# Kernel tuning notes

Measured on AMD Instinct MI355X. Metric: run time of the kernel, lower is better.

## Reference

```python
import jax, jax.numpy as jnp
import numpy as np

B, LMAX, NCOND, NHID = 256, 512, 300, 600

def setup_inputs() -> dict:
    key = jax.random.key(0)
    ks = jax.random.split(key, 7)
    x = jax.random.normal(ks[0], (B, NCOND), dtype=jnp.float32)
    context = jax.random.normal(ks[1], (B, LMAX, NCOND), dtype=jnp.float32)
    lengths = jax.random.randint(ks[2], (B,), 0, LMAX, dtype=jnp.int32)
    W1 = jax.random.normal(ks[3], (NCOND, NHID), dtype=jnp.float32) * (1.0 / np.sqrt(NCOND))
    b1 = jax.random.normal(ks[4], (NHID,), dtype=jnp.float32) * 0.02
    Wa = jax.random.normal(ks[5], (NHID, NCOND), dtype=jnp.float32) * (1.0 / np.sqrt(NHID))
    ba = jax.random.normal(ks[6], (NCOND,), dtype=jnp.float32) * 0.02
    return {"x": x, "context": context, "lengths": lengths, "W1": W1, "b1": b1, "Wa": Wa, "ba": ba}

def reference(x, context, lengths, W1, b1, Wa, ba):
    # lengths clamped to >=1 (a ragged context is always non-empty)
    lens = jnp.maximum(lengths, 1)
    # valid-position mask over padded context: [B, L, 1]
    valid = (jnp.arange(LMAX)[None, :] < lens[:, None])[..., None].astype(context.dtype)
    # per-token MLP: relu(ctx @ W1 + b1)  -> [B, L, nhid]
    h = jax.nn.relu(jnp.einsum('blc,ch->blh', context, W1) + b1)
    # masked mean over valid tokens (ragged mean-pool) -> [B, nhid]
    pooled = jnp.sum(h * valid, axis=1) / lens[:, None].astype(context.dtype)
    # sigmoid gate -> [B, ncond], applied to x embeddings
    gate = jax.nn.sigmoid(jnp.einsum('bh,hc->bc', pooled, Wa) + ba)
    return gate * x
```

## Files before the change

### kernel.cpp

```cpp
#include <hip/hip_runtime.h>
#include <math.h>

#define BB     256
#define LMAX   512
#define NCOND  300
#define NHID   600
#define NSEG   8
#define CHUNK  64
#define KPAD   320
#define KLDS   328
#define NKC    10

#define AS1 __attribute__((address_space(1)))
#define AS3 __attribute__((address_space(3)))

typedef short s16x8 __attribute__((ext_vector_type(8)));
typedef float f32x4 __attribute__((ext_vector_type(4)));
typedef unsigned short u16x4 __attribute__((ext_vector_type(4)));

__device__ inline unsigned short f2bf(float f) {
    unsigned int x = __float_as_uint(f);
    x += 0x7fffu + ((x >> 16) & 1u);
    return (unsigned short)(x >> 16);
}

__global__ __launch_bounds__(256) void k0_w1t(const float* __restrict__ W1,
                                              unsigned short* __restrict__ w1t)
{
    const int t     = blockIdx.x * 256 + threadIdx.x;
    const int lane  = t & 63;
    const int g     = t >> 6;
    const int ntile = g / NKC;
    const int kc    = g - ntile * NKC;
    const int n     = ntile * 16 + (lane & 15);
    const int kbase = kc * 32 + (lane >> 4) * 8;
    union { unsigned short us[8]; s16x8 v8; } u;
#pragma unroll
    for (int j = 0; j < 8; ++j) {
        const int k = kbase + j;
        const float w = (n < NHID && k < NCOND) ? W1[(size_t)k * NHID + n] : 0.f;
        u.us[j] = f2bf(w);
    }
    *(s16x8*)(w1t + (size_t)t * 8) = u.v8;
}

__global__ __launch_bounds__(256) void k0b_cvt(const float* __restrict__ ctx,
                                               const int* __restrict__ lengths,
                                               unsigned short* __restrict__ ctx16)
{
    const int b = blockIdx.x, s = blockIdx.y, tid = threadIdx.x;
    int count = lengths[b]; if (count < 1) count = 1;
    if (s * CHUNK >= count) return;

    const size_t inbase  = ((size_t)b * LMAX + s * CHUNK) * NCOND;
    const float* src = ctx + inbase;
    char* dst = (char*)(ctx16 + ((size_t)b * LMAX + s * CHUNK) * KPAD);

#pragma unroll
    for (int i = 0; i < 20; ++i) {
        const int c   = i * 256 + tid;
        const int row = c / 80;
        const int q   = c - row * 80;
        float4 v = make_float4(0.f, 0.f, 0.f, 0.f);
        if (q < 75)
            v = *(const float4*)(src + (size_t)row * NCOND + q * 4);
        union { unsigned short us[4]; u16x4 v4; } o;
        o.us[0] = f2bf(v.x); o.us[1] = f2bf(v.y);
        o.us[2] = f2bf(v.z); o.us[3] = f2bf(v.w);
        const int off = (row * 640 + q * 8) ^ ((row & 7) << 4);
        *(u16x4*)(dst + off) = o.v4;
    }
}

__global__ __launch_bounds__(256, 3) void k1_mfma_dma(
    const unsigned short* __restrict__ ctx16, const int* __restrict__ lengths,
    const unsigned short* __restrict__ w1t, const float* __restrict__ b1,
    float* __restrict__ partial)
{
    const int b  = blockIdx.x;
    const int s  = blockIdx.y;
    const int ch = blockIdx.z;

    int count = lengths[b]; if (count < 1) count = 1;
    const int l0 = s * CHUNK;
    if (l0 >= count) return;
    const int valid = min(count - l0, CHUNK);

    const int tid  = threadIdx.x;
    const int lane = tid & 63;
    const int wv   = tid >> 6;
    const int ln15 = lane & 15;
    const int kg   = lane >> 4;

    __shared__ __align__(16) unsigned short atile[CHUNK * KPAD];

    const char* gsrc = (const char*)(ctx16 + ((size_t)b * LMAX + l0) * KPAD);
    char* lbase = (char*)atile;
#pragma unroll
    for (int r = 0; r < 10; ++r) {
        const int off = (r * 4 + wv) * 1024;
        __builtin_amdgcn_global_load_lds(
            (const AS1 void*)(gsrc + off + lane * 16),
            (AS3 void*)(lbase + off),
            16, 0, 0);
    }

    const int ntile0 = ch * 20 + wv * 5;
    const unsigned short* bbase = w1t + ((size_t)ntile0 * NKC * 64 + lane) * 8;
    s16x8 bf[2][5];
#pragma unroll
    for (int nt = 0; nt < 5; ++nt) bf[0][nt] = *(const s16x8*)(bbase + nt * 5120);

    __syncthreads();

    const int swz   = (ln15 & 7) << 4;
    const int abase = ln15 * 640 + kg * 16;
    const char* ab  = (const char*)atile;

    f32x4 acc[5][4];
#pragma unroll
    for (int nt = 0; nt < 5; ++nt)
#pragma unroll
        for (int mt = 0; mt < 4; ++mt) acc[nt][mt] = (f32x4){0.f, 0.f, 0.f, 0.f};

#pragma unroll
    for (int kc = 0; kc < NKC; ++kc) {
        const int cur = kc & 1, nxt = cur ^ 1;
        if (kc < NKC - 1) {
#pragma unroll
            for (int nt = 0; nt < 5; ++nt)
                bf[nxt][nt] = *(const s16x8*)(bbase + nt * 5120 + (kc + 1) * 512);
        }
        s16x8 af[4];
#pragma unroll
        for (int mt = 0; mt < 4; ++mt)
            af[mt] = *(const s16x8*)(ab + ((abase + mt * 10240 + kc * 64) ^ swz));
#pragma unroll
        for (int nt = 0; nt < 5; ++nt)
#pragma unroll
            for (int mt = 0; mt < 4; ++mt)
                acc[nt][mt] = __builtin_amdgcn_mfma_f32_16x16x32_bf16(
                    af[mt], bf[cur][nt], acc[nt][mt], 0, 0, 0);
    }

#pragma unroll
    for (int nt = 0; nt < 5; ++nt) {
        const int colg = ch * 320 + wv * 80 + nt * 16 + ln15;
        const float b1c = (colg < NHID) ? b1[colg] : 0.f;
        float ssum = 0.f;
#pragma unroll
        for (int mt = 0; mt < 4; ++mt) {
            const int rbase = mt * 16 + kg * 4;
#pragma unroll
            for (int r = 0; r < 4; ++r) {
                const float h = fmaxf(acc[nt][mt][r] + b1c, 0.f);
                if (rbase + r < valid) ssum += h;
            }
        }
        ssum += __shfl_xor(ssum, 16, 64);
        ssum += __shfl_xor(ssum, 32, 64);
        if (kg == 0 && colg < NHID)
            partial[((size_t)s * BB + b) * NHID + colg] = ssum;
    }
}

__global__ __launch_bounds__(256, 3) void k1_mfma_pool(
    const float* __restrict__ ctx, const int* __restrict__ lengths,
    const unsigned short* __restrict__ w1t, const float* __restrict__ b1,
    float* __restrict__ partial)
{
    const int b  = blockIdx.x;
    const int s  = blockIdx.y;
    const int ch = blockIdx.z;

    int count = lengths[b]; if (count < 1) count = 1;
    const int l0 = s * CHUNK;
    if (l0 >= count) return;
    const int valid = min(count - l0, CHUNK);

    const int tid  = threadIdx.x;
    const int lane = tid & 63;
    const int wv   = tid >> 6;
    const int ln15 = lane & 15;
    const int kg   = lane >> 4;

    __shared__ __align__(16) unsigned short atile[CHUNK * KLDS];

#pragma unroll
    for (int p = 0; p < 10; ++p) {
        const int i  = p * 256 + tid;
        const int r  = i / 40;
        const int c8 = i - r * 40;
        union { unsigned short us[8]; s16x8 v8; } u;
        if (r < valid && c8 < 38) {
            const float* src = ctx + ((size_t)b * LMAX + l0 + r) * NCOND + c8 * 8;
            const float4 v0 = *(const float4*)src;
            float4 v1 = make_float4(0.f, 0.f, 0.f, 0.f);
            if (c8 < 37) v1 = *(const float4*)(src + 4);
            u.us[0] = f2bf(v0.x); u.us[1] = f2bf(v0.y);
            u.us[2] = f2bf(v0.z); u.us[3] = f2bf(v0.w);
            u.us[4] = f2bf(v1.x); u.us[5] = f2bf(v1.y);
            u.us[6] = f2bf(v1.z); u.us[7] = f2bf(v1.w);
        } else {
#pragma unroll
            for (int j = 0; j < 8; ++j) u.us[j] = 0;
        }
        *(s16x8*)(atile + r * KLDS + c8 * 8) = u.v8;
    }
    __syncthreads();

    const int ntile0 = ch * 20 + wv * 5;
    const unsigned short* bbase = w1t + ((size_t)ntile0 * NKC * 64 + lane) * 8;
    const unsigned short* arow  = atile + ln15 * KLDS + kg * 8;

    f32x4 acc[5][4];
#pragma unroll
    for (int nt = 0; nt < 5; ++nt)
#pragma unroll
        for (int mt = 0; mt < 4; ++mt) acc[nt][mt] = (f32x4){0.f, 0.f, 0.f, 0.f};

    s16x8 bf[2][5];
#pragma unroll
    for (int nt = 0; nt < 5; ++nt) bf[0][nt] = *(const s16x8*)(bbase + nt * 5120);

#pragma unroll
    for (int kc = 0; kc < NKC; ++kc) {
        const int cur = kc & 1, nxt = cur ^ 1;
        if (kc < NKC - 1) {
#pragma unroll
            for (int nt = 0; nt < 5; ++nt)
                bf[nxt][nt] = *(const s16x8*)(bbase + nt * 5120 + (kc + 1) * 512);
        }
        s16x8 af[4];
#pragma unroll
        for (int mt = 0; mt < 4; ++mt)
            af[mt] = *(const s16x8*)(arow + mt * 16 * KLDS + kc * 32);
#pragma unroll
        for (int nt = 0; nt < 5; ++nt)
#pragma unroll
            for (int mt = 0; mt < 4; ++mt)
                acc[nt][mt] = __builtin_amdgcn_mfma_f32_16x16x32_bf16(
                    af[mt], bf[cur][nt], acc[nt][mt], 0, 0, 0);
    }

#pragma unroll
    for (int nt = 0; nt < 5; ++nt) {
        const int colg = ch * 320 + wv * 80 + nt * 16 + ln15;
        const float b1c = (colg < NHID) ? b1[colg] : 0.f;
        float ssum = 0.f;
#pragma unroll
        for (int mt = 0; mt < 4; ++mt) {
            const int rbase = mt * 16 + kg * 4;
#pragma unroll
            for (int r = 0; r < 4; ++r) {
                const float h = fmaxf(acc[nt][mt][r] + b1c, 0.f);
                if (rbase + r < valid) ssum += h;
            }
        }
        ssum += __shfl_xor(ssum, 16, 64);
        ssum += __shfl_xor(ssum, 32, 64);
        if (kg == 0 && colg < NHID)
            partial[((size_t)s * BB + b) * NHID + colg] = ssum;
    }
}

__global__ __launch_bounds__(640) void k2_gate(
    const float* __restrict__ x, const int* __restrict__ lengths,
    const float* __restrict__ partial, const float* __restrict__ Wa,
    const float* __restrict__ ba, float* __restrict__ out)
{
    const int b0  = blockIdx.x * 2;
    const int tid = threadIdx.x;

    __shared__ float pl[2][NHID];

    if (tid < NHID) {
#pragma unroll
        for (int bb = 0; bb < 2; ++bb) {
            int count = lengths[b0 + bb]; if (count < 1) count = 1;
            const int nch = (count + CHUNK - 1) >> 6;
            float ssum = 0.f;
            for (int sp = 0; sp < nch; ++sp)
                ssum += partial[((size_t)sp * BB + (b0 + bb)) * NHID + tid];
            pl[bb][tid] = ssum / (float)count;
        }
    }
    __syncthreads();

    if (tid < 2 * NCOND) {
        const int bb = tid / NCOND;
        const int n  = tid - bb * NCOND;
        const int b  = b0 + bb;
        float a0 = ba[n], a1 = 0.f, a2 = 0.f, a3 = 0.f;
        const float4* p4 = (const float4*)pl[bb];
        for (int h4 = 0; h4 < 148; h4 += 4) {
            const float4 pv0 = p4[h4];
            const float4 pv1 = p4[h4 + 1];
            const float4 pv2 = p4[h4 + 2];
            const float4 pv3 = p4[h4 + 3];
            const int hb = h4 * 4;
            a0 = fmaf(pv0.x, Wa[(size_t)(hb +  0) * NCOND + n], a0);
            a0 = fmaf(pv0.y, Wa[(size_t)(hb +  1) * NCOND + n], a0);
            a0 = fmaf(pv0.z, Wa[(size_t)(hb +  2) * NCOND + n], a0);
            a0 = fmaf(pv0.w, Wa[(size_t)(hb +  3) * NCOND + n], a0);
            a1 = fmaf(pv1.x, Wa[(size_t)(hb +  4) * NCOND + n], a1);
            a1 = fmaf(pv1.y, Wa[(size_t)(hb +  5) * NCOND + n], a1);
            a1 = fmaf(pv1.z, Wa[(size_t)(hb +  6) * NCOND + n], a1);
            a1 = fmaf(pv1.w, Wa[(size_t)(hb +  7) * NCOND + n], a1);
            a2 = fmaf(pv2.x, Wa[(size_t)(hb +  8) * NCOND + n], a2);
            a2 = fmaf(pv2.y, Wa[(size_t)(hb +  9) * NCOND + n], a2);
            a2 = fmaf(pv2.z, Wa[(size_t)(hb + 10) * NCOND + n], a2);
            a2 = fmaf(pv2.w, Wa[(size_t)(hb + 11) * NCOND + n], a2);
            a3 = fmaf(pv3.x, Wa[(size_t)(hb + 12) * NCOND + n], a3);
            a3 = fmaf(pv3.y, Wa[(size_t)(hb + 13) * NCOND + n], a3);
            a3 = fmaf(pv3.z, Wa[(size_t)(hb + 14) * NCOND + n], a3);
            a3 = fmaf(pv3.w, Wa[(size_t)(hb + 15) * NCOND + n], a3);
        }
        {
            const float4 pv0 = p4[148];
            const float4 pv1 = p4[149];
            a0 = fmaf(pv0.x, Wa[(size_t)592 * NCOND + n], a0);
            a0 = fmaf(pv0.y, Wa[(size_t)593 * NCOND + n], a0);
            a0 = fmaf(pv0.z, Wa[(size_t)594 * NCOND + n], a0);
            a0 = fmaf(pv0.w, Wa[(size_t)595 * NCOND + n], a0);
            a1 = fmaf(pv1.x, Wa[(size_t)596 * NCOND + n], a1);
            a1 = fmaf(pv1.y, Wa[(size_t)597 * NCOND + n], a1);
            a1 = fmaf(pv1.z, Wa[(size_t)598 * NCOND + n], a1);
            a1 = fmaf(pv1.w, Wa[(size_t)599 * NCOND + n], a1);
        }
        const float acc  = (a0 + a1) + (a2 + a3);
        const float gate = 1.0f / (1.0f + expf(-acc));
        out[(size_t)b * NCOND + n] = gate * x[(size_t)b * NCOND + n];
    }
}

extern "C" void kernel_launch(void* const* d_in, const int* in_sizes, int n_in,
                              void* d_out, int out_size, void* d_ws, size_t ws_size,
                              hipStream_t stream)
{
    const float* x       = (const float*)d_in[0];
    const float* ctx     = (const float*)d_in[1];
    const int*   lengths = (const int*)  d_in[2];
    const float* W1      = (const float*)d_in[3];
    const float* b1      = (const float*)d_in[4];
    const float* Wa      = (const float*)d_in[5];
    const float* ba      = (const float*)d_in[6];
    float*       out     = (float*)d_out;

    const size_t W1T_B   = 409600;
    const size_t PART_B  = 4915200;
    const size_t CTX16_B = (size_t)BB * LMAX * KPAD * 2;
    const size_t NEED    = W1T_B + PART_B + CTX16_B;

    unsigned short* w1t     = (unsigned short*)d_ws;
    float*          partial = (float*)((char*)d_ws + W1T_B);

    k0_w1t<<<100, 256, 0, stream>>>(W1, w1t);

    if (ws_size >= NEED) {
        unsigned short* ctx16 = (unsigned short*)((char*)d_ws + W1T_B + PART_B);
        k0b_cvt<<<dim3(BB, NSEG), 256, 0, stream>>>(ctx, lengths, ctx16);
        k1_mfma_dma<<<dim3(BB, NSEG, 2), 256, 0, stream>>>(ctx16, lengths, w1t, b1, partial);
    } else {
        k1_mfma_pool<<<dim3(BB, NSEG, 2), 256, 0, stream>>>(ctx, lengths, w1t, b1, partial);
    }

    k2_gate<<<BB / 2, 640, 0, stream>>>(x, lengths, partial, Wa, ba, out);
}
```

Before: 309.5 us.

## Use one persistent block per batch with double-buffered segment DMA

Replaces the per-(batch, segment, column-half) MFMA kernel with a 512-thread block per batch row. Each block loops over that row's valid 64-token segments, prefetching the next bf16 segment into a second LDS buffer while it computes the current one, and keeps the pooled sums in registers. Because each block now writes only a single pooled vector, the partial buffer shrinks and the gate kernel no longer sums per-segment partials. The conversion kernel also switches to 8-wide loads and stores. The cost is far fewer blocks with uneven work: rows with long lengths run up to 8 segments serially, and W1 fragments are reloaded for every segment.

```diff
diff --git a/kernel.cpp b/kernel.cpp
--- a/kernel.cpp
+++ b/kernel.cpp
@@ -10,13 +10,14 @@
 #define KPAD   320
 #define KLDS   328
 #define NKC    10
+#define SEGB   (CHUNK * KPAD * 2)
 
 #define AS1 __attribute__((address_space(1)))
 #define AS3 __attribute__((address_space(3)))
 
 typedef short s16x8 __attribute__((ext_vector_type(8)));
 typedef float f32x4 __attribute__((ext_vector_type(4)));
-typedef unsigned short u16x4 __attribute__((ext_vector_type(4)));
+typedef unsigned short u16x8 __attribute__((ext_vector_type(8)));
 
 __device__ inline unsigned short f2bf(float f) {
     unsigned int x = __float_as_uint(f);
@@ -52,39 +53,37 @@
     int count = lengths[b]; if (count < 1) count = 1;
     if (s * CHUNK >= count) return;
 
-    const size_t inbase  = ((size_t)b * LMAX + s * CHUNK) * NCOND;
-    const float* src = ctx + inbase;
+    const float* src = ctx + ((size_t)b * LMAX + s * CHUNK) * NCOND;
     char* dst = (char*)(ctx16 + ((size_t)b * LMAX + s * CHUNK) * KPAD);
 
 #pragma unroll
-    for (int i = 0; i < 20; ++i) {
+    for (int i = 0; i < 10; ++i) {
         const int c   = i * 256 + tid;
-        const int row = c / 80;
-        const int q   = c - row * 80;
-        float4 v = make_float4(0.f, 0.f, 0.f, 0.f);
-        if (q < 75)
-            v = *(const float4*)(src + (size_t)row * NCOND + q * 4);
-        union { unsigned short us[4]; u16x4 v4; } o;
-        o.us[0] = f2bf(v.x); o.us[1] = f2bf(v.y);
-        o.us[2] = f2bf(v.z); o.us[3] = f2bf(v.w);
-        const int off = (row * 640 + q * 8) ^ ((row & 7) << 4);
-        *(u16x4*)(dst + off) = o.v4;
-    }
-}
-
-__global__ __launch_bounds__(256, 3) void k1_mfma_dma(
+        const int row = c / 40;
+        const int q2  = c - row * 40;
+        float4 v0 = make_float4(0.f, 0.f, 0.f, 0.f);
+        float4 v1 = make_float4(0.f, 0.f, 0.f, 0.f);
+        const float* rsrc = src + (size_t)row * NCOND + q2 * 8;
+        if (q2 < 38) v0 = *(const float4*)rsrc;
+        if (q2 < 37) v1 = *(const float4*)(rsrc + 4);
+        union { unsigned short us[8]; u16x8 v8; } o;
+        o.us[0] = f2bf(v0.x); o.us[1] = f2bf(v0.y);
+        o.us[2] = f2bf(v0.z); o.us[3] = f2bf(v0.w);
+        o.us[4] = f2bf(v1.x); o.us[5] = f2bf(v1.y);
+        o.us[6] = f2bf(v1.z); o.us[7] = f2bf(v1.w);
+        const int off = (row * 640 + q2 * 16) ^ ((row & 7) << 4);
+        *(u16x8*)(dst + off) = o.v8;
+    }
+}
+
+__global__ __launch_bounds__(512, 2) void k1_persist(
     const unsigned short* __restrict__ ctx16, const int* __restrict__ lengths,
     const unsigned short* __restrict__ w1t, const float* __restrict__ b1,
     float* __restrict__ partial)
 {
-    const int b  = blockIdx.x;
-    const int s  = blockIdx.y;
-    const int ch = blockIdx.z;
-
+    const int b = blockIdx.x;
     int count = lengths[b]; if (count < 1) count = 1;
-    const int l0 = s * CHUNK;
-    if (l0 >= count) return;
-    const int valid = min(count - l0, CHUNK);
+    const int nseg = (count + CHUNK - 1) >> 6;
 
     const int tid  = threadIdx.x;
     const int lane = tid & 63;
@@ -92,179 +91,109 @@
     const int ln15 = lane & 15;
     const int kg   = lane >> 4;
 
-    __shared__ __align__(16) unsigned short atile[CHUNK * KPAD];
-
-    const char* gsrc = (const char*)(ctx16 + ((size_t)b * LMAX + l0) * KPAD);
-    char* lbase = (char*)atile;
-#pragma unroll
-    for (int r = 0; r < 10; ++r) {
-        const int off = (r * 4 + wv) * 1024;
+    __shared__ __align__(16) unsigned short atile[2][CHUNK * KPAD];
+
+    float bq[5];
+#pragma unroll
+    for (int nt = 0; nt < 5; ++nt) {
+        const int colg = wv * 80 + nt * 16 + ln15;
+        bq[nt] = (colg < NHID) ? b1[colg] : 0.f;
+    }
+
+    const unsigned short* bbase = w1t + ((size_t)(wv * 5) * NKC * 64 + lane) * 8;
+    const char* gseg = (const char*)(ctx16 + (size_t)b * LMAX * KPAD);
+
+#pragma unroll
+    for (int r = 0; r < 5; ++r) {
+        const int off = (r * 8 + wv) * 1024;
         __builtin_amdgcn_global_load_lds(
-            (const AS1 void*)(gsrc + off + lane * 16),
-            (AS3 void*)(lbase + off),
-            16, 0, 0);
-    }
-
-    const int ntile0 = ch * 20 + wv * 5;
-    const unsigned short* bbase = w1t + ((size_t)ntile0 * NKC * 64 + lane) * 8;
-    s16x8 bf[2][5];
-#pragma unroll
-    for (int nt = 0; nt < 5; ++nt) bf[0][nt] = *(const s16x8*)(bbase + nt * 5120);
-
-    __syncthreads();
-
+            (const AS1 void*)(gseg + off + lane * 16),
+            (AS3 void*)((char*)atile[0] + off), 16, 0, 0);
+    }
+
+    float ssum[5] = {0.f, 0.f, 0.f, 0.f, 0.f};
     const int swz   = (ln15 & 7) << 4;
     const int abase = ln15 * 640 + kg * 16;
-    const char* ab  = (const char*)atile;
-
-    f32x4 acc[5][4];
-#pragma unroll
-    for (int nt = 0; nt < 5; ++nt)
-#pragma unroll
-        for (int mt = 0; mt < 4; ++mt) acc[nt][mt] = (f32x4){0.f, 0.f, 0.f, 0.f};
-
-#pragma unroll
-    for (int kc = 0; kc < NKC; ++kc) {
-        const int cur = kc & 1, nxt = cur ^ 1;
-        if (kc < NKC - 1) {
+
+    __syncthreads();
+
+    for (int s = 0; s < nseg; ++s) {
+        const int cur = s & 1;
+
+        if (s + 1 < nseg) {
+            const char* gnext = gseg + (size_t)(s + 1) * SEGB;
+#pragma unroll
+            for (int r = 0; r < 5; ++r) {
+                const int off = (r * 8 + wv) * 1024;
+                __builtin_amdgcn_global_load_lds(
+                    (const AS1 void*)(gnext + off + lane * 16),
+                    (AS3 void*)((char*)atile[cur ^ 1] + off), 16, 0, 0);
+            }
+        }
+
+        const char* ab = (const char*)atile[cur];
+
+        f32x4 acc[5][4];
+#pragma unroll
+        for (int nt = 0; nt < 5; ++nt)
+#pragma unroll
+            for (int mt = 0; mt < 4; ++mt) acc[nt][mt] = (f32x4){0.f, 0.f, 0.f, 0.f};
+
+        s16x8 bf[2][5];
+#pragma unroll
+        for (int nt = 0; nt < 5; ++nt) bf[0][nt] = *(const s16x8*)(bbase + nt * 5120);
+
+#pragma unroll
+        for (int kc = 0; kc < NKC; ++kc) {
+            const int curk = kc & 1, nxtk = curk ^ 1;
+            if (kc < NKC - 1) {
+#pragma unroll
+                for (int nt = 0; nt < 5; ++nt)
+                    bf[nxtk][nt] = *(const s16x8*)(bbase + nt * 5120 + (kc + 1) * 512);
+            }
+            s16x8 af[4];
+#pragma unroll
+            for (int mt = 0; mt < 4; ++mt)
+                af[mt] = *(const s16x8*)(ab + ((abase + mt * 10240 + kc * 64) ^ swz));
 #pragma unroll
             for (int nt = 0; nt < 5; ++nt)
-                bf[nxt][nt] = *(const s16x8*)(bbase + nt * 5120 + (kc + 1) * 512);
-        }
-        s16x8 af[4];
-#pragma unroll
-        for (int mt = 0; mt < 4; ++mt)
-            af[mt] = *(const s16x8*)(ab + ((abase + mt * 10240 + kc * 64) ^ swz));
-#pragma unroll
-        for (int nt = 0; nt < 5; ++nt)
-#pragma unroll
-            for (int mt = 0; mt < 4; ++mt)
-                acc[nt][mt] = __builtin_amdgcn_mfma_f32_16x16x32_bf16(
-                    af[mt], bf[cur][nt], acc[nt][mt], 0, 0, 0);
+#pragma unroll
+                for (int mt = 0; mt < 4; ++mt)
+                    acc[nt][mt] = __builtin_amdgcn_mfma_f32_16x16x32_bf16(
+                        af[mt], bf[curk][nt], acc[nt][mt], 0, 0, 0);
+        }
+
+        const int valid = min(count - s * CHUNK, CHUNK);
+#pragma unroll
+        for (int nt = 0; nt < 5; ++nt) {
+            float t = 0.f;
+#pragma unroll
+            for (int mt = 0; mt < 4; ++mt) {
+                const int rbase = mt * 16 + kg * 4;
+#pragma unroll
+                for (int r = 0; r < 4; ++r) {
+                    const float h = fmaxf(acc[nt][mt][r] + bq[nt], 0.f);
+                    if (rbase + r < valid) t += h;
+                }
+            }
+            ssum[nt] += t;
+        }
+
+        __syncthreads();
     }
 
 #pragma unroll
     for (int nt = 0; nt < 5; ++nt) {
-        const int colg = ch * 320 + wv * 80 + nt * 16 + ln15;
-        const float b1c = (colg < NHID) ? b1[colg] : 0.f;
-        float ssum = 0.f;
-#pragma unroll
-        for (int mt = 0; mt < 4; ++mt) {
-            const int rbase = mt * 16 + kg * 4;
-#pragma unroll
-            for (int r = 0; r < 4; ++r) {
-                const float h = fmaxf(acc[nt][mt][r] + b1c, 0.f);
-                if (rbase + r < valid) ssum += h;
-            }
-        }
-        ssum += __shfl_xor(ssum, 16, 64);
-        ssum += __shfl_xor(ssum, 32, 64);
+        float v = ssum[nt];
+        v += __shfl_xor(v, 16, 64);
+        v += __shfl_xor(v, 32, 64);
+        const int colg = wv * 80 + nt * 16 + ln15;
         if (kg == 0 && colg < NHID)
-            partial[((size_t)s * BB + b) * NHID + colg] = ssum;
-    }
-}
-
-__global__ __launch_bounds__(256, 3) void k1_mfma_pool(
-    const float* __restrict__ ctx, const int* __restrict__ lengths,
-    const unsigned short* __restrict__ w1t, const float* __restrict__ b1,
-    float* __restrict__ partial)
-{
-    const int b  = blockIdx.x;
-    const int s  = blockIdx.y;
-    const int ch = blockIdx.z;
-
-    int count = lengths[b]; if (count < 1) count = 1;
-    const int l0 = s * CHUNK;
-    if (l0 >= count) return;
-    const int valid = min(count - l0, CHUNK);
-
-    const int tid  = threadIdx.x;
-    const int lane = tid & 63;
-    const int wv   = tid >> 6;
-    const int ln15 = lane & 15;
-    const int kg   = lane >> 4;
-
-    __shared__ __align__(16) unsigned short atile[CHUNK * KLDS];
-
-#pragma unroll
-    for (int p = 0; p < 10; ++p) {
-        const int i  = p * 256 + tid;
-        const int r  = i / 40;
-        const int c8 = i - r * 40;
-        union { unsigned short us[8]; s16x8 v8; } u;
-        if (r < valid && c8 < 38) {
-            const float* src = ctx + ((size_t)b * LMAX + l0 + r) * NCOND + c8 * 8;
-            const float4 v0 = *(const float4*)src;
-            float4 v1 = make_float4(0.f, 0.f, 0.f, 0.f);
-            if (c8 < 37) v1 = *(const float4*)(src + 4);
-            u.us[0] = f2bf(v0.x); u.us[1] = f2bf(v0.y);
-            u.us[2] = f2bf(v0.z); u.us[3] = f2bf(v0.w);
-            u.us[4] = f2bf(v1.x); u.us[5] = f2bf(v1.y);
-            u.us[6] = f2bf(v1.z); u.us[7] = f2bf(v1.w);
-        } else {
-#pragma unroll
-            for (int j = 0; j < 8; ++j) u.us[j] = 0;
-        }
-        *(s16x8*)(atile + r * KLDS + c8 * 8) = u.v8;
-    }
-    __syncthreads();
-
-    const int ntile0 = ch * 20 + wv * 5;
-    const unsigned short* bbase = w1t + ((size_t)ntile0 * NKC * 64 + lane) * 8;
-    const unsigned short* arow  = atile + ln15 * KLDS + kg * 8;
-
-    f32x4 acc[5][4];
-#pragma unroll
-    for (int nt = 0; nt < 5; ++nt)
-#pragma unroll
-        for (int mt = 0; mt < 4; ++mt) acc[nt][mt] = (f32x4){0.f, 0.f, 0.f, 0.f};
-
-    s16x8 bf[2][5];
-#pragma unroll
-    for (int nt = 0; nt < 5; ++nt) bf[0][nt] = *(const s16x8*)(bbase + nt * 5120);
-
-#pragma unroll
-    for (int kc = 0; kc < NKC; ++kc) {
-        const int cur = kc & 1, nxt = cur ^ 1;
-        if (kc < NKC - 1) {
-#pragma unroll
-            for (int nt = 0; nt < 5; ++nt)
-                bf[nxt][nt] = *(const s16x8*)(bbase + nt * 5120 + (kc + 1) * 512);
-        }
-        s16x8 af[4];
-#pragma unroll
-        for (int mt = 0; mt < 4; ++mt)
-            af[mt] = *(const s16x8*)(arow + mt * 16 * KLDS + kc * 32);
-#pragma unroll
-        for (int nt = 0; nt < 5; ++nt)
-#pragma unroll
-            for (int mt = 0; mt < 4; ++mt)
-                acc[nt][mt] = __builtin_amdgcn_mfma_f32_16x16x32_bf16(
-                    af[mt], bf[cur][nt], acc[nt][mt], 0, 0, 0);
-    }
-
-#pragma unroll
-    for (int nt = 0; nt < 5; ++nt) {
-        const int colg = ch * 320 + wv * 80 + nt * 16 + ln15;
-        const float b1c = (colg < NHID) ? b1[colg] : 0.f;
-        float ssum = 0.f;
-#pragma unroll
-        for (int mt = 0; mt < 4; ++mt) {
-            const int rbase = mt * 16 + kg * 4;
-#pragma unroll
-            for (int r = 0; r < 4; ++r) {
-                const float h = fmaxf(acc[nt][mt][r] + b1c, 0.f);
-                if (rbase + r < valid) ssum += h;
-            }
-        }
-        ssum += __shfl_xor(ssum, 16, 64);
-        ssum += __shfl_xor(ssum, 32, 64);
-        if (kg == 0 && colg < NHID)
-            partial[((size_t)s * BB + b) * NHID + colg] = ssum;
-    }
-}
-
-__global__ __launch_bounds__(640) void k2_gate(
+            partial[(size_t)b * NHID + colg] = v;
+    }
+}
+
+__global__ __launch_bounds__(640) void k2_gate2(
     const float* __restrict__ x, const int* __restrict__ lengths,
     const float* __restrict__ partial, const float* __restrict__ Wa,
     const float* __restrict__ ba, float* __restrict__ out)
@@ -278,11 +207,7 @@
 #pragma unroll
         for (int bb = 0; bb < 2; ++bb) {
             int count = lengths[b0 + bb]; if (count < 1) count = 1;
-            const int nch = (count + CHUNK - 1) >> 6;
-            float ssum = 0.f;
-            for (int sp = 0; sp < nch; ++sp)
-                ssum += partial[((size_t)sp * BB + (b0 + bb)) * NHID + tid];
-            pl[bb][tid] = ssum / (float)count;
+            pl[bb][tid] = partial[(size_t)(b0 + bb) * NHID + tid] / (float)count;
         }
     }
     __syncthreads();
@@ -334,6 +259,176 @@
     }
 }
 
+__global__ __launch_bounds__(256, 3) void k1_mfma_pool(
+    const float* __restrict__ ctx, const int* __restrict__ lengths,
+    const unsigned short* __restrict__ w1t, const float* __restrict__ b1,
+    float* __restrict__ partial)
+{
+    const int b  = blockIdx.x;
+    const int s  = blockIdx.y;
+    const int ch = blockIdx.z;
+
+    int count = lengths[b]; if (count < 1) count = 1;
+    const int l0 = s * CHUNK;
+    if (l0 >= count) return;
+    const int valid = min(count - l0, CHUNK);
+
+    const int tid  = threadIdx.x;
+    const int lane = tid & 63;
+    const int wv   = tid >> 6;
+    const int ln15 = lane & 15;
+    const int kg   = lane >> 4;
+
+    __shared__ __align__(16) unsigned short atile[CHUNK * KLDS];
+
+#pragma unroll
+    for (int p = 0; p < 10; ++p) {
+        const int i  = p * 256 + tid;
+        const int r  = i / 40;
+        const int c8 = i - r * 40;
+        union { unsigned short us[8]; s16x8 v8; } u;
+        if (r < valid && c8 < 38) {
+            const float* src = ctx + ((size_t)b * LMAX + l0 + r) * NCOND + c8 * 8;
+            const float4 v0 = *(const float4*)src;
+            float4 v1 = make_float4(0.f, 0.f, 0.f, 0.f);
+            if (c8 < 37) v1 = *(const float4*)(src + 4);
+            u.us[0] = f2bf(v0.x); u.us[1] = f2bf(v0.y);
+            u.us[2] = f2bf(v0.z); u.us[3] = f2bf(v0.w);
+            u.us[4] = f2bf(v1.x); u.us[5] = f2bf(v1.y);
+            u.us[6] = f2bf(v1.z); u.us[7] = f2bf(v1.w);
+        } else {
+#pragma unroll
+            for (int j = 0; j < 8; ++j) u.us[j] = 0;
+        }
+        *(s16x8*)(atile + r * KLDS + c8 * 8) = u.v8;
+    }
+    __syncthreads();
+
+    const int ntile0 = ch * 20 + wv * 5;
+    const unsigned short* bbase = w1t + ((size_t)ntile0 * NKC * 64 + lane) * 8;
+    const unsigned short* arow  = atile + ln15 * KLDS + kg * 8;
+
+    f32x4 acc[5][4];
+#pragma unroll
+    for (int nt = 0; nt < 5; ++nt)
+#pragma unroll
+        for (int mt = 0; mt < 4; ++mt) acc[nt][mt] = (f32x4){0.f, 0.f, 0.f, 0.f};
+
+    s16x8 bf[2][5];
+#pragma unroll
+    for (int nt = 0; nt < 5; ++nt) bf[0][nt] = *(const s16x8*)(bbase + nt * 5120);
+
+#pragma unroll
+    for (int kc = 0; kc < NKC; ++kc) {
+        const int cur = kc & 1, nxt = cur ^ 1;
+        if (kc < NKC - 1) {
+#pragma unroll
+            for (int nt = 0; nt < 5; ++nt)
+                bf[nxt][nt] = *(const s16x8*)(bbase + nt * 5120 + (kc + 1) * 512);
+        }
+        s16x8 af[4];
+#pragma unroll
+        for (int mt = 0; mt < 4; ++mt)
+            af[mt] = *(const s16x8*)(arow + mt * 16 * KLDS + kc * 32);
+#pragma unroll
+        for (int nt = 0; nt < 5; ++nt)
+#pragma unroll
+            for (int mt = 0; mt < 4; ++mt)
+                acc[nt][mt] = __builtin_amdgcn_mfma_f32_16x16x32_bf16(
+                    af[mt], bf[cur][nt], acc[nt][mt], 0, 0, 0);
+    }
+
+#pragma unroll
+    for (int nt = 0; nt < 5; ++nt) {
+        const int colg = ch * 320 + wv * 80 + nt * 16 + ln15;
+        const float b1c = (colg < NHID) ? b1[colg] : 0.f;
+        float ssum = 0.f;
+#pragma unroll
+        for (int mt = 0; mt < 4; ++mt) {
+            const int rbase = mt * 16 + kg * 4;
+#pragma unroll
+            for (int r = 0; r < 4; ++r) {
+                const float h = fmaxf(acc[nt][mt][r] + b1c, 0.f);
+                if (rbase + r < valid) ssum += h;
+            }
+        }
+        ssum += __shfl_xor(ssum, 16, 64);
+        ssum += __shfl_xor(ssum, 32, 64);
+        if (kg == 0 && colg < NHID)
+            partial[((size_t)s * BB + b) * NHID + colg] = ssum;
+    }
+}
+
+__global__ __launch_bounds__(640) void k2_gate(
+    const float* __restrict__ x, const int* __restrict__ lengths,
+    const float* __restrict__ partial, const float* __restrict__ Wa,
+    const float* __restrict__ ba, float* __restrict__ out)
+{
+    const int b0  = blockIdx.x * 2;
+    const int tid = threadIdx.x;
+
+    __shared__ float pl[2][NHID];
+
+    if (tid < NHID) {
+#pragma unroll
+        for (int bb = 0; bb < 2; ++bb) {
+            int count = lengths[b0 + bb]; if (count < 1) count = 1;
+            const int nch = (count + CHUNK - 1) >> 6;
+            float ssum = 0.f;
+            for (int sp = 0; sp < nch; ++sp)
+                ssum += partial[((size_t)sp * BB + (b0 + bb)) * NHID + tid];
+            pl[bb][tid] = ssum / (float)count;
+        }
+    }
+    __syncthreads();
+
+    if (tid < 2 * NCOND) {
+        const int bb = tid / NCOND;
+        const int n  = tid - bb * NCOND;
+        const int b  = b0 + bb;
+        float a0 = ba[n], a1 = 0.f, a2 = 0.f, a3 = 0.f;
+        const float4* p4 = (const float4*)pl[bb];
+        for (int h4 = 0; h4 < 148; h4 += 4) {
+            const float4 pv0 = p4[h4];
+            const float4 pv1 = p4[h4 + 1];
+            const float4 pv2 = p4[h4 + 2];
+            const float4 pv3 = p4[h4 + 3];
+            const int hb = h4 * 4;
+            a0 = fmaf(pv0.x, Wa[(size_t)(hb +  0) * NCOND + n], a0);
+            a0 = fmaf(pv0.y, Wa[(size_t)(hb +  1) * NCOND + n], a0);
+            a0 = fmaf(pv0.z, Wa[(size_t)(hb +  2) * NCOND + n], a0);
+            a0 = fmaf(pv0.w, Wa[(size_t)(hb +  3) * NCOND + n], a0);
+            a1 = fmaf(pv1.x, Wa[(size_t)(hb +  4) * NCOND + n], a1);
+            a1 = fmaf(pv1.y, Wa[(size_t)(hb +  5) * NCOND + n], a1);
+            a1 = fmaf(pv1.z, Wa[(size_t)(hb +  6) * NCOND + n], a1);
+            a1 = fmaf(pv1.w, Wa[(size_t)(hb +  7) * NCOND + n], a1);
+            a2 = fmaf(pv2.x, Wa[(size_t)(hb +  8) * NCOND + n], a2);
+            a2 = fmaf(pv2.y, Wa[(size_t)(hb +  9) * NCOND + n], a2);
+            a2 = fmaf(pv2.z, Wa[(size_t)(hb + 10) * NCOND + n], a2);
+            a2 = fmaf(pv2.w, Wa[(size_t)(hb + 11) * NCOND + n], a2);
+            a3 = fmaf(pv3.x, Wa[(size_t)(hb + 12) * NCOND + n], a3);
+            a3 = fmaf(pv3.y, Wa[(size_t)(hb + 13) * NCOND + n], a3);
+            a3 = fmaf(pv3.z, Wa[(size_t)(hb + 14) * NCOND + n], a3);
+            a3 = fmaf(pv3.w, Wa[(size_t)(hb + 15) * NCOND + n], a3);
+        }
+        {
+            const float4 pv0 = p4[148];
+            const float4 pv1 = p4[149];
+            a0 = fmaf(pv0.x, Wa[(size_t)592 * NCOND + n], a0);
+            a0 = fmaf(pv0.y, Wa[(size_t)593 * NCOND + n], a0);
+            a0 = fmaf(pv0.z, Wa[(size_t)594 * NCOND + n], a0);
+            a0 = fmaf(pv0.w, Wa[(size_t)595 * NCOND + n], a0);
+            a1 = fmaf(pv1.x, Wa[(size_t)596 * NCOND + n], a1);
+            a1 = fmaf(pv1.y, Wa[(size_t)597 * NCOND + n], a1);
+            a1 = fmaf(pv1.z, Wa[(size_t)598 * NCOND + n], a1);
+            a1 = fmaf(pv1.w, Wa[(size_t)599 * NCOND + n], a1);
+        }
+        const float acc  = (a0 + a1) + (a2 + a3);
+        const float gate = 1.0f / (1.0f + expf(-acc));
+        out[(size_t)b * NCOND + n] = gate * x[(size_t)b * NCOND + n];
+    }
+}
+
 extern "C" void kernel_launch(void* const* d_in, const int* in_sizes, int n_in,
                               void* d_out, int out_size, void* d_ws, size_t ws_size,
                               hipStream_t stream)
@@ -348,7 +443,7 @@
     float*       out     = (float*)d_out;
 
     const size_t W1T_B   = 409600;
-    const size_t PART_B  = 4915200;
+    const size_t PART_B  = 614400;
     const size_t CTX16_B = (size_t)BB * LMAX * KPAD * 2;
     const size_t NEED    = W1T_B + PART_B + CTX16_B;
 
@@ -360,10 +455,10 @@
     if (ws_size >= NEED) {
         unsigned short* ctx16 = (unsigned short*)((char*)d_ws + W1T_B + PART_B);
         k0b_cvt<<<dim3(BB, NSEG), 256, 0, stream>>>(ctx, lengths, ctx16);
-        k1_mfma_dma<<<dim3(BB, NSEG, 2), 256, 0, stream>>>(ctx16, lengths, w1t, b1, partial);
+        k1_persist<<<BB, 512, 0, stream>>>(ctx16, lengths, w1t, b1, partial);
+        k2_gate2<<<BB / 2, 640, 0, stream>>>(x, lengths, partial, Wa, ba, out);
     } else {
         k1_mfma_pool<<<dim3(BB, NSEG, 2), 256, 0, stream>>>(ctx, lengths, w1t, b1, partial);
-    }
-
-    k2_gate<<<BB / 2, 640, 0, stream>>>(x, lengths, partial, Wa, ba, out);
-}
+        k2_gate<<<BB / 2, 640, 0, stream>>>(x, lengths, partial, Wa, ba, out);
+    }
+}
```

Measured after the change: 379.9 us. 22.8% more time.

## Pre-swizzle context into MFMA fragment layout and load A directly from global

Applied to the files above, without the earlier changes.

The conversion kernel now writes bf16 context in the exact per-lane MFMA fragment order, so the GEMM kernel can load A operands straight from global memory into registers with double buffering. This drops the LDS staging, the async global-to-LDS copy and the block barrier. The grid order is changed so the two column-half blocks of one (batch, segment) tile run next to each other and can share the tile through L2, and launch bounds drop to 2 blocks per SIMD to leave room for the extra A registers. The cost is more global/L2 traffic per wave and lower occupancy.

```diff
diff --git a/kernel.cpp b/kernel.cpp
--- a/kernel.cpp
+++ b/kernel.cpp
@@ -10,13 +10,11 @@
 #define KPAD   320
 #define KLDS   328
 #define NKC    10
-
-#define AS1 __attribute__((address_space(1)))
-#define AS3 __attribute__((address_space(3)))
+#define TILE16 20480
 
 typedef short s16x8 __attribute__((ext_vector_type(8)));
 typedef float f32x4 __attribute__((ext_vector_type(4)));
-typedef unsigned short u16x4 __attribute__((ext_vector_type(4)));
+typedef unsigned short u16x8 __attribute__((ext_vector_type(8)));
 
 __device__ inline unsigned short f2bf(float f) {
     unsigned int x = __float_as_uint(f);
@@ -44,42 +42,46 @@
     *(s16x8*)(w1t + (size_t)t * 8) = u.v8;
 }
 
-__global__ __launch_bounds__(256) void k0b_cvt(const float* __restrict__ ctx,
-                                               const int* __restrict__ lengths,
-                                               unsigned short* __restrict__ ctx16)
+__global__ __launch_bounds__(256) void k0b_frag(const float* __restrict__ ctx,
+                                                const int* __restrict__ lengths,
+                                                unsigned short* __restrict__ ctx16)
 {
     const int b = blockIdx.x, s = blockIdx.y, tid = threadIdx.x;
     int count = lengths[b]; if (count < 1) count = 1;
     if (s * CHUNK >= count) return;
 
-    const size_t inbase  = ((size_t)b * LMAX + s * CHUNK) * NCOND;
-    const float* src = ctx + inbase;
-    char* dst = (char*)(ctx16 + ((size_t)b * LMAX + s * CHUNK) * KPAD);
-
-#pragma unroll
-    for (int i = 0; i < 20; ++i) {
-        const int c   = i * 256 + tid;
-        const int row = c / 80;
-        const int q   = c - row * 80;
-        float4 v = make_float4(0.f, 0.f, 0.f, 0.f);
-        if (q < 75)
-            v = *(const float4*)(src + (size_t)row * NCOND + q * 4);
-        union { unsigned short us[4]; u16x4 v4; } o;
-        o.us[0] = f2bf(v.x); o.us[1] = f2bf(v.y);
-        o.us[2] = f2bf(v.z); o.us[3] = f2bf(v.w);
-        const int off = (row * 640 + q * 8) ^ ((row & 7) << 4);
-        *(u16x4*)(dst + off) = o.v4;
-    }
-}
-
-__global__ __launch_bounds__(256, 3) void k1_mfma_dma(
+    const float* src = ctx + ((size_t)b * LMAX + s * CHUNK) * NCOND;
+    unsigned short* dst = ctx16 + (size_t)(b * NSEG + s) * TILE16;
+
+#pragma unroll
+    for (int p = 0; p < 10; ++p) {
+        const int i   = p * 256 + tid;
+        const int row = i / 40;
+        const int q   = i - row * 40;
+        float4 v0 = make_float4(0.f, 0.f, 0.f, 0.f);
+        float4 v1 = make_float4(0.f, 0.f, 0.f, 0.f);
+        const float* rsrc = src + (size_t)row * NCOND + q * 8;
+        if (q < 38) v0 = *(const float4*)rsrc;
+        if (q < 37) v1 = *(const float4*)(rsrc + 4);
+        union { unsigned short us[8]; u16x8 v8; } o;
+        o.us[0] = f2bf(v0.x); o.us[1] = f2bf(v0.y);
+        o.us[2] = f2bf(v0.z); o.us[3] = f2bf(v0.w);
+        o.us[4] = f2bf(v1.x); o.us[5] = f2bf(v1.y);
+        o.us[6] = f2bf(v1.z); o.us[7] = f2bf(v1.w);
+        const int mt = row >> 4, kc = q >> 2;
+        const int lane = ((q & 3) << 4) + (row & 15);
+        *(u16x8*)(dst + (((mt * NKC + kc) * 64 + lane) << 3)) = o.v8;
+    }
+}
+
+__global__ __launch_bounds__(256, 2) void k1_direct(
     const unsigned short* __restrict__ ctx16, const int* __restrict__ lengths,
     const unsigned short* __restrict__ w1t, const float* __restrict__ b1,
     float* __restrict__ partial)
 {
-    const int b  = blockIdx.x;
+    const int ch = blockIdx.x;
     const int s  = blockIdx.y;
-    const int ch = blockIdx.z;
+    const int b  = blockIdx.z;
 
     int count = lengths[b]; if (count < 1) count = 1;
     const int l0 = s * CHUNK;
@@ -92,155 +94,38 @@
     const int ln15 = lane & 15;
     const int kg   = lane >> 4;
 
-    __shared__ __align__(16) unsigned short atile[CHUNK * KPAD];
-
-    const char* gsrc = (const char*)(ctx16 + ((size_t)b * LMAX + l0) * KPAD);
-    char* lbase = (char*)atile;
-#pragma unroll
-    for (int r = 0; r < 10; ++r) {
-        const int off = (r * 4 + wv) * 1024;
-        __builtin_amdgcn_global_load_lds(
-            (const AS1 void*)(gsrc + off + lane * 16),
-            (AS3 void*)(lbase + off),
-            16, 0, 0);
-    }
-
-    const int ntile0 = ch * 20 + wv * 5;
-    const unsigned short* bbase = w1t + ((size_t)ntile0 * NKC * 64 + lane) * 8;
-    s16x8 bf[2][5];
+    const unsigned short* abase = ctx16 + (size_t)(b * NSEG + s) * TILE16 + (size_t)lane * 8;
+    const unsigned short* bbase = w1t + ((size_t)(ch * 20 + wv * 5) * NKC * 64 + lane) * 8;
+
+    f32x4 acc[5][4];
+#pragma unroll
+    for (int nt = 0; nt < 5; ++nt)
+#pragma unroll
+        for (int mt = 0; mt < 4; ++mt) acc[nt][mt] = (f32x4){0.f, 0.f, 0.f, 0.f};
+
+    s16x8 af[2][4], bf[2][5];
+#pragma unroll
+    for (int mt = 0; mt < 4; ++mt) af[0][mt] = *(const s16x8*)(abase + mt * 5120);
 #pragma unroll
     for (int nt = 0; nt < 5; ++nt) bf[0][nt] = *(const s16x8*)(bbase + nt * 5120);
-
-    __syncthreads();
-
-    const int swz   = (ln15 & 7) << 4;
-    const int abase = ln15 * 640 + kg * 16;
-    const char* ab  = (const char*)atile;
-
-    f32x4 acc[5][4];
-#pragma unroll
-    for (int nt = 0; nt < 5; ++nt)
-#pragma unroll
-        for (int mt = 0; mt < 4; ++mt) acc[nt][mt] = (f32x4){0.f, 0.f, 0.f, 0.f};
 
 #pragma unroll
     for (int kc = 0; kc < NKC; ++kc) {
         const int cur = kc & 1, nxt = cur ^ 1;
         if (kc < NKC - 1) {
 #pragma unroll
+            for (int mt = 0; mt < 4; ++mt)
+                af[nxt][mt] = *(const s16x8*)(abase + mt * 5120 + (kc + 1) * 512);
+#pragma unroll
             for (int nt = 0; nt < 5; ++nt)
                 bf[nxt][nt] = *(const s16x8*)(bbase + nt * 5120 + (kc + 1) * 512);
         }
-        s16x8 af[4];
-#pragma unroll
-        for (int mt = 0; mt < 4; ++mt)
-            af[mt] = *(const s16x8*)(ab + ((abase + mt * 10240 + kc * 64) ^ swz));
 #pragma unroll
         for (int nt = 0; nt < 5; ++nt)
 #pragma unroll
             for (int mt = 0; mt < 4; ++mt)
                 acc[nt][mt] = __builtin_amdgcn_mfma_f32_16x16x32_bf16(
-                    af[mt], bf[cur][nt], acc[nt][mt], 0, 0, 0);
-    }
-
-#pragma unroll
-    for (int nt = 0; nt < 5; ++nt) {
-        const int colg = ch * 320 + wv * 80 + nt * 16 + ln15;
-        const float b1c = (colg < NHID) ? b1[colg] : 0.f;
-        float ssum = 0.f;
-#pragma unroll
-        for (int mt = 0; mt < 4; ++mt) {
-            const int rbase = mt * 16 + kg * 4;
-#pragma unroll
-            for (int r = 0; r < 4; ++r) {
-                const float h = fmaxf(acc[nt][mt][r] + b1c, 0.f);
-                if (rbase + r < valid) ssum += h;
-            }
-        }
-        ssum += __shfl_xor(ssum, 16, 64);
-        ssum += __shfl_xor(ssum, 32, 64);
-        if (kg == 0 && colg < NHID)
-            partial[((size_t)s * BB + b) * NHID + colg] = ssum;
-    }
-}
-
-__global__ __launch_bounds__(256, 3) void k1_mfma_pool(
-    const float* __restrict__ ctx, const int* __restrict__ lengths,
-    const unsigned short* __restrict__ w1t, const float* __restrict__ b1,
-    float* __restrict__ partial)
-{
-    const int b  = blockIdx.x;
-    const int s  = blockIdx.y;
-    const int ch = blockIdx.z;
-
-    int count = lengths[b]; if (count < 1) count = 1;
-    const int l0 = s * CHUNK;
-    if (l0 >= count) return;
-    const int valid = min(count - l0, CHUNK);
-
-    const int tid  = threadIdx.x;
-    const int lane = tid & 63;
-    const int wv   = tid >> 6;
-    const int ln15 = lane & 15;
-    const int kg   = lane >> 4;
-
-    __shared__ __align__(16) unsigned short atile[CHUNK * KLDS];
-
-#pragma unroll
-    for (int p = 0; p < 10; ++p) {
-        const int i  = p * 256 + tid;
-        const int r  = i / 40;
-        const int c8 = i - r * 40;
-        union { unsigned short us[8]; s16x8 v8; } u;
-        if (r < valid && c8 < 38) {
-            const float* src = ctx + ((size_t)b * LMAX + l0 + r) * NCOND + c8 * 8;
-            const float4 v0 = *(const float4*)src;
-            float4 v1 = make_float4(0.f, 0.f, 0.f, 0.f);
-            if (c8 < 37) v1 = *(const float4*)(src + 4);
-            u.us[0] = f2bf(v0.x); u.us[1] = f2bf(v0.y);
-            u.us[2] = f2bf(v0.z); u.us[3] = f2bf(v0.w);
-            u.us[4] = f2bf(v1.x); u.us[5] = f2bf(v1.y);
-            u.us[6] = f2bf(v1.z); u.us[7] = f2bf(v1.w);
-        } else {
-#pragma unroll
-            for (int j = 0; j < 8; ++j) u.us[j] = 0;
-        }
-        *(s16x8*)(atile + r * KLDS + c8 * 8) = u.v8;
-    }
-    __syncthreads();
-
-    const int ntile0 = ch * 20 + wv * 5;
-    const unsigned short* bbase = w1t + ((size_t)ntile0 * NKC * 64 + lane) * 8;
-    const unsigned short* arow  = atile + ln15 * KLDS + kg * 8;
-
-    f32x4 acc[5][4];
-#pragma unroll
-    for (int nt = 0; nt < 5; ++nt)
-#pragma unroll
-        for (int mt = 0; mt < 4; ++mt) acc[nt][mt] = (f32x4){0.f, 0.f, 0.f, 0.f};
-
-    s16x8 bf[2][5];
-#pragma unroll
-    for (int nt = 0; nt < 5; ++nt) bf[0][nt] = *(const s16x8*)(bbase + nt * 5120);
-
-#pragma unroll
-    for (int kc = 0; kc < NKC; ++kc) {
-        const int cur = kc & 1, nxt = cur ^ 1;
-        if (kc < NKC - 1) {
-#pragma unroll
-            for (int nt = 0; nt < 5; ++nt)
-                bf[nxt][nt] = *(const s16x8*)(bbase + nt * 5120 + (kc + 1) * 512);
-        }
-        s16x8 af[4];
-#pragma unroll
-        for (int mt = 0; mt < 4; ++mt)
-            af[mt] = *(const s16x8*)(arow + mt * 16 * KLDS + kc * 32);
-#pragma unroll
-        for (int nt = 0; nt < 5; ++nt)
-#pragma unroll
-            for (int mt = 0; mt < 4; ++mt)
-                acc[nt][mt] = __builtin_amdgcn_mfma_f32_16x16x32_bf16(
-                    af[mt], bf[cur][nt], acc[nt][mt], 0, 0, 0);
+                    af[cur][mt], bf[cur][nt], acc[nt][mt], 0, 0, 0);
     }
 
 #pragma unroll
@@ -334,6 +219,106 @@
     }
 }
 
+__global__ __launch_bounds__(256, 3) void k1_mfma_pool(
+    const float* __restrict__ ctx, const int* __restrict__ lengths,
+    const unsigned short* __restrict__ w1t, const float* __restrict__ b1,
+    float* __restrict__ partial)
+{
+    const int b  = blockIdx.x;
+    const int s  = blockIdx.y;
+    const int ch = blockIdx.z;
+
+    int count = lengths[b]; if (count < 1) count = 1;
+    const int l0 = s * CHUNK;
+    if (l0 >= count) return;
+    const int valid = min(count - l0, CHUNK);
+
+    const int tid  = threadIdx.x;
+    const int lane = tid & 63;
+    const int wv   = tid >> 6;
+    const int ln15 = lane & 15;
+    const int kg   = lane >> 4;
+
+    __shared__ __align__(16) unsigned short atile[CHUNK * KLDS];
+
+#pragma unroll
+    for (int p = 0; p < 10; ++p) {
+        const int i  = p * 256 + tid;
+        const int r  = i / 40;
+        const int c8 = i - r * 40;
+        union { unsigned short us[8]; s16x8 v8; } u;
+        if (r < valid && c8 < 38) {
+            const float* src = ctx + ((size_t)b * LMAX + l0 + r) * NCOND + c8 * 8;
+            const float4 v0 = *(const float4*)src;
+            float4 v1 = make_float4(0.f, 0.f, 0.f, 0.f);
+            if (c8 < 37) v1 = *(const float4*)(src + 4);
+            u.us[0] = f2bf(v0.x); u.us[1] = f2bf(v0.y);
+            u.us[2] = f2bf(v0.z); u.us[3] = f2bf(v0.w);
+            u.us[4] = f2bf(v1.x); u.us[5] = f2bf(v1.y);
+            u.us[6] = f2bf(v1.z); u.us[7] = f2bf(v1.w);
+        } else {
+#pragma unroll
+            for (int j = 0; j < 8; ++j) u.us[j] = 0;
+        }
+        *(s16x8*)(atile + r * KLDS + c8 * 8) = u.v8;
+    }
+    __syncthreads();
+
+    const int ntile0 = ch * 20 + wv * 5;
+    const unsigned short* bbase = w1t + ((size_t)ntile0 * NKC * 64 + lane) * 8;
+    const unsigned short* arow  = atile + ln15 * KLDS + kg * 8;
+
+    f32x4 acc[5][4];
+#pragma unroll
+    for (int nt = 0; nt < 5; ++nt)
+#pragma unroll
+        for (int mt = 0; mt < 4; ++mt) acc[nt][mt] = (f32x4){0.f, 0.f, 0.f, 0.f};
+
+    s16x8 bf[2][5];
+#pragma unroll
+    for (int nt = 0; nt < 5; ++nt) bf[0][nt] = *(const s16x8*)(bbase + nt * 5120);
+
+#pragma unroll
+    for (int kc = 0; kc < NKC; ++kc) {
+        const int cur = kc & 1, nxt = cur ^ 1;
+        if (kc < NKC - 1) {
+#pragma unroll
+            for (int nt = 0; nt < 5; ++nt)
+                bf[nxt][nt] = *(const s16x8*)(bbase + nt * 5120 + (kc + 1) * 512);
+        }
+        s16x8 af[4];
+#pragma unroll
+        for (int mt = 0; mt < 4; ++mt)
+            af[mt] = *(const s16x8*)(arow + mt * 16 * KLDS + kc * 32);
+#pragma unroll
+        for (int nt = 0; nt < 5; ++nt)
+#pragma unroll
+            for (int mt = 0; mt < 4; ++mt)
+                acc[nt][mt] = __builtin_amdgcn_mfma_f32_16x16x32_bf16(
+                    af[mt], bf[cur][nt], acc[nt][mt], 0, 0, 0);
+    }
+
+#pragma unroll
+    for (int nt = 0; nt < 5; ++nt) {
+        const int colg = ch * 320 + wv * 80 + nt * 16 + ln15;
+        const float b1c = (colg < NHID) ? b1[colg] : 0.f;
+        float ssum = 0.f;
+#pragma unroll
+        for (int mt = 0; mt < 4; ++mt) {
+            const int rbase = mt * 16 + kg * 4;
+#pragma unroll
+            for (int r = 0; r < 4; ++r) {
+                const float h = fmaxf(acc[nt][mt][r] + b1c, 0.f);
+                if (rbase + r < valid) ssum += h;
+            }
+        }
+        ssum += __shfl_xor(ssum, 16, 64);
+        ssum += __shfl_xor(ssum, 32, 64);
+        if (kg == 0 && colg < NHID)
+            partial[((size_t)s * BB + b) * NHID + colg] = ssum;
+    }
+}
+
 extern "C" void kernel_launch(void* const* d_in, const int* in_sizes, int n_in,
                               void* d_out, int out_size, void* d_ws, size_t ws_size,
                               hipStream_t stream)
@@ -349,7 +334,7 @@
 
     const size_t W1T_B   = 409600;
     const size_t PART_B  = 4915200;
-    const size_t CTX16_B = (size_t)BB * LMAX * KPAD * 2;
+    const size_t CTX16_B = (size_t)BB * NSEG * TILE16 * 2;
     const size_t NEED    = W1T_B + PART_B + CTX16_B;
 
     unsigned short* w1t     = (unsigned short*)d_ws;
@@ -359,8 +344,8 @@
 
     if (ws_size >= NEED) {
         unsigned short* ctx16 = (unsigned short*)((char*)d_ws + W1T_B + PART_B);
-        k0b_cvt<<<dim3(BB, NSEG), 256, 0, stream>>>(ctx, lengths, ctx16);
-        k1_mfma_dma<<<dim3(BB, NSEG, 2), 256, 0, stream>>>(ctx16, lengths, w1t, b1, partial);
+        k0b_frag<<<dim3(BB, NSEG), 256, 0, stream>>>(ctx, lengths, ctx16);
+        k1_direct<<<dim3(2, NSEG, BB), 256, 0, stream>>>(ctx16, lengths, w1t, b1, partial);
     } else {
         k1_mfma_pool<<<dim3(BB, NSEG, 2), 256, 0, stream>>>(ctx, lengths, w1t, b1, partial);
     }
```

Result: slower. 368.5 us (+19.0%).
